# Kernel tuning notes

Measured on AMD Instinct MI355X. Metric: run time of the kernel, lower is better.

The kernel has to match this reference:

```python
import jax, jax.numpy as jnp
import numpy as np

HIDDEN = 100

def _lstm_step(h, c, gx, Whh, bhh):
    # gx: precomputed input contribution W_ih @ x + b_ih, shape [4H]
    gates = gx + Whh @ h + bhh
    i, f, g, o = jnp.split(gates, 4)
    i = jax.nn.sigmoid(i)
    f = jax.nn.sigmoid(f)
    g = jnp.tanh(g)
    o = jax.nn.sigmoid(o)
    c = f * c + i * g
    h = o * jnp.tanh(c)
    return h, c


def setup_inputs() -> dict:
    key = jax.random.key(0)
    ks = jax.random.split(key, 12)
    s = 0.1
    T_enc, T_dec = 4096, 4096
    return {
        "x": jax.random.normal(ks[0], (1, T_enc, 3), jnp.float32),
        "y": jax.random.randint(ks[1], (1, T_dec), 0, 6),
        "enc_Wih": jax.random.normal(ks[2], (4 * HIDDEN, 3), jnp.float32) * s,
        "enc_Whh": jax.random.normal(ks[3], (4 * HIDDEN, HIDDEN), jnp.float32) * s,
        "enc_bih": jax.random.normal(ks[4], (4 * HIDDEN,), jnp.float32) * s,
        "enc_bhh": jax.random.normal(ks[5], (4 * HIDDEN,), jnp.float32) * s,
        "dec_Wih": jax.random.normal(ks[6], (4 * HIDDEN, 1), jnp.float32) * s,
        "dec_Whh": jax.random.normal(ks[7], (4 * HIDDEN, HIDDEN), jnp.float32) * s,
        "dec_bih": jax.random.normal(ks[8], (4 * HIDDEN,), jnp.float32) * s,
        "dec_bhh": jax.random.normal(ks[9], (4 * HIDDEN,), jnp.float32) * s,
        "lin_W": jax.random.normal(ks[10], (6, HIDDEN), jnp.float32) * s,
        "lin_b": jax.random.normal(ks[11], (6,), jnp.float32) * s,
        "teacher_forcing_ratio": 1,
        "n_classes": 6,
    }


def reference(x, y, enc_Wih, enc_Whh, enc_bih, enc_bhh,
              dec_Wih, dec_Whh, dec_bih, dec_bhh, lin_W, lin_b,
              teacher_forcing_ratio, n_classes):
    T_dec = y.shape[1]
    # ---- Encoder: batch=1 LSTM over source sequence ----
    gx_enc = x[0] @ enc_Wih.T + enc_bih  # [T_enc, 4H]

    def enc_step(carry, gx):
        h, c = carry
        h, c = _lstm_step(h, c, gx, enc_Whh, enc_bhh)
        return (h, c), None

    h0 = jnp.zeros((HIDDEN,), x.dtype)
    (h_enc, c_enc), _ = jax.lax.scan(enc_step, (h0, h0), gx_enc)

    # ---- Decoder: single-step loop with teacher forcing ----
    yf = y[0].astype(jnp.float32)          # target labels fed as floats
    ratio = jnp.float32(teacher_forcing_ratio)
    u = jax.random.uniform(jax.random.key(1), (T_dec - 1,), jnp.float32)

    def dec_step(carry, inp):
        h, c, dec_in = carry
        u_t, y_t = inp
        gx = dec_in * dec_Wih[:, 0] + dec_bih  # scalar input -> [4H]
        h, c = _lstm_step(h, c, gx, dec_Whh, dec_bhh)
        logits = lin_W @ h + lin_b             # [n_classes]
        top_pred = jnp.argmax(logits).astype(jnp.float32)
        new_in = jnp.where(u_t < ratio, y_t, top_pred)
        return (h, c, new_in), logits

    _, logits_seq = jax.lax.scan(dec_step, (h_enc, c_enc, yf[0]), (u, yf[1:]))
    # outputs[0][t-1] = logits at step t, t = 1..T_dec-1; last row stays zero
    outputs = jnp.zeros((1, T_dec, n_classes), jnp.float32)
    outputs = outputs.at[0, : T_dec - 1].set(logits_seq)
    return outputs
```

## Files before the change

### kernel.cpp

```cpp
#include <hip/hip_runtime.h>

typedef _Float16 h2_t __attribute__((ext_vector_type(2)));

#define HID  100
#define TENC 4096
#define TDEC 4096
#define NCLS 6
#define NTHR 256

__device__ __forceinline__ float sigm(float v)  { return __builtin_amdgcn_rcpf(1.0f + __expf(-v)); }
__device__ __forceinline__ float tanh_(float v) { return 1.0f - 2.0f * __builtin_amdgcn_rcpf(1.0f + __expf(2.0f * v)); }

#define SYNC_LDS() asm volatile("s_waitcnt lgkmcnt(0)\n\ts_barrier" ::: "memory")

__device__ __forceinline__ float packh2(float a, float b) {
    h2_t p; p[0] = (_Float16)a; p[1] = (_Float16)b;
    return __builtin_bit_cast(float, p);
}

__global__ __launch_bounds__(NTHR, 1)
void lstm_rec(const float* __restrict__ x,
              const int*   __restrict__ y,
              const float* __restrict__ eWih,
              const float* __restrict__ eWhh,
              const float* __restrict__ ebih,
              const float* __restrict__ ebhh,
              const float* __restrict__ dWih,
              const float* __restrict__ dWhh,
              const float* __restrict__ dbih,
              const float* __restrict__ dbhh,
              float* __restrict__ hsto)
{
    __shared__ __align__(16) _Float16 hbuf[2][2][64];
    __shared__ __align__(8)  uint2    xst[TENC];
    __shared__               unsigned yst[TDEC];

    const int  t    = threadIdx.x;
    const int  w    = t >> 6;
    const int  l    = t & 63;
    const int  ci   = l & 31;
    const int  half = l >> 5;
    const int  cell = w * 32 + ci;
    const bool live = (cell < HID);
    const int  k0   = half * 50;

    for (int i = t; i < TENC; i += NTHR) {
        const float a = x[3*i], b = x[3*i+1], cc = x[3*i+2];
        uint2 u;
        u.x = __builtin_bit_cast(unsigned, packh2(a, b));
        u.y = __builtin_bit_cast(unsigned, packh2(cc, 1.0f));
        xst[i] = u;
    }
    for (int i = t; i < TDEC; i += NTHR)
        yst[i] = __builtin_bit_cast(unsigned, packh2((float)y[i], 0.0f));
    if (t < 256) ((_Float16*)hbuf)[t] = (_Float16)0.0f;

    float wf[4][25];
    float wxp[4][2], bs[4];
    float c = 0.0f;
    #pragma unroll
    for (int r = 0; r < 4; ++r) {
        #pragma unroll
        for (int j = 0; j < 25; ++j) wf[r][j] = 0.0f;
        wxp[r][0] = wxp[r][1] = 0.0f; bs[r] = 0.0f;
    }
    if (live) {
        #pragma unroll
        for (int r = 0; r < 4; ++r) {
            const int row = cell + r * HID;
            #pragma unroll
            for (int j = 0; j < 25; ++j)
                wf[r][j] = packh2(eWhh[row*HID + k0 + 2*j], eWhh[row*HID + k0 + 2*j + 1]);
            if (half == 0) {
                wxp[r][0] = packh2(eWih[row*3+0], eWih[row*3+1]);
                wxp[r][1] = packh2(eWih[row*3+2], 0.0f);
                bs[r]     = ebih[row] + ebhh[row];
            }
        }
    }
    __syncthreads();

    int p = 0;

    for (int s = 0; s < TENC; ++s) {
        const float4* h4 = (const float4*)&hbuf[p][half][0];
        float hp[25];
        #pragma unroll
        for (int j = 0; j < 6; ++j) {
            const float4 v = h4[j];
            hp[4*j+0] = v.x; hp[4*j+1] = v.y; hp[4*j+2] = v.z; hp[4*j+3] = v.w;
        }
        hp[24] = ((const float*)h4)[24];

        float a0, a1, a2, a3;
        if (half == 0) {
            const uint2 xp = xst[s];
            const h2_t x0 = __builtin_bit_cast(h2_t, xp.x);
            const h2_t x1 = __builtin_bit_cast(h2_t, xp.y);
            a0 = __builtin_amdgcn_fdot2(__builtin_bit_cast(h2_t, wxp[0][0]), x0,
                 __builtin_amdgcn_fdot2(__builtin_bit_cast(h2_t, wxp[0][1]), x1, bs[0], false), false);
            a1 = __builtin_amdgcn_fdot2(__builtin_bit_cast(h2_t, wxp[1][0]), x0,
                 __builtin_amdgcn_fdot2(__builtin_bit_cast(h2_t, wxp[1][1]), x1, bs[1], false), false);
            a2 = __builtin_amdgcn_fdot2(__builtin_bit_cast(h2_t, wxp[2][0]), x0,
                 __builtin_amdgcn_fdot2(__builtin_bit_cast(h2_t, wxp[2][1]), x1, bs[2], false), false);
            a3 = __builtin_amdgcn_fdot2(__builtin_bit_cast(h2_t, wxp[3][0]), x0,
                 __builtin_amdgcn_fdot2(__builtin_bit_cast(h2_t, wxp[3][1]), x1, bs[3], false), false);
        } else { a0 = a1 = a2 = a3 = 0.0f; }

        #pragma unroll
        for (int j = 0; j < 25; ++j) {
            const h2_t hh = __builtin_bit_cast(h2_t, hp[j]);
            a0 = __builtin_amdgcn_fdot2(__builtin_bit_cast(h2_t, wf[0][j]), hh, a0, false);
            a1 = __builtin_amdgcn_fdot2(__builtin_bit_cast(h2_t, wf[1][j]), hh, a1, false);
            a2 = __builtin_amdgcn_fdot2(__builtin_bit_cast(h2_t, wf[2][j]), hh, a2, false);
            a3 = __builtin_amdgcn_fdot2(__builtin_bit_cast(h2_t, wf[3][j]), hh, a3, false);
        }
        a0 += __shfl_xor(a0, 32);
        a1 += __shfl_xor(a1, 32);
        a2 += __shfl_xor(a2, 32);
        a3 += __shfl_xor(a3, 32);

        const float fi = sigm(a0), ff = sigm(a1), fg = tanh_(a2), fo = sigm(a3);
        c = ff * c + fi * fg;
        const float hn = fo * tanh_(c);
        if (half == 0 && live) {
            const int hh2 = (cell < 50) ? 0 : 1;
            hbuf[p ^ 1][hh2][cell - 50*hh2] = (_Float16)hn;
        }
        SYNC_LDS();
        p ^= 1;
    }

    float wdp[4], bsd[4];
    #pragma unroll
    for (int r = 0; r < 4; ++r) { wdp[r] = 0.0f; bsd[r] = 0.0f; }
    if (live) {
        #pragma unroll
        for (int r = 0; r < 4; ++r) {
            const int row = cell + r * HID;
            #pragma unroll
            for (int j = 0; j < 25; ++j)
                wf[r][j] = packh2(dWhh[row*HID + k0 + 2*j], dWhh[row*HID + k0 + 2*j + 1]);
            if (half == 0) {
                wdp[r] = packh2(dWih[row], 0.0f);
                bsd[r] = dbih[row] + dbhh[row];
            }
        }
    }

    for (int s = 0; s < TDEC - 1; ++s) {
        const float4* h4 = (const float4*)&hbuf[p][half][0];
        float hp[25];
        #pragma unroll
        for (int j = 0; j < 6; ++j) {
            const float4 v = h4[j];
            hp[4*j+0] = v.x; hp[4*j+1] = v.y; hp[4*j+2] = v.z; hp[4*j+3] = v.w;
        }
        hp[24] = ((const float*)h4)[24];

        float a0, a1, a2, a3;
        if (half == 0) {
            const h2_t yp = __builtin_bit_cast(h2_t, yst[s]);
            a0 = __builtin_amdgcn_fdot2(__builtin_bit_cast(h2_t, wdp[0]), yp, bsd[0], false);
            a1 = __builtin_amdgcn_fdot2(__builtin_bit_cast(h2_t, wdp[1]), yp, bsd[1], false);
            a2 = __builtin_amdgcn_fdot2(__builtin_bit_cast(h2_t, wdp[2]), yp, bsd[2], false);
            a3 = __builtin_amdgcn_fdot2(__builtin_bit_cast(h2_t, wdp[3]), yp, bsd[3], false);
        } else { a0 = a1 = a2 = a3 = 0.0f; }

        #pragma unroll
        for (int j = 0; j < 25; ++j) {
            const h2_t hh = __builtin_bit_cast(h2_t, hp[j]);
            a0 = __builtin_amdgcn_fdot2(__builtin_bit_cast(h2_t, wf[0][j]), hh, a0, false);
            a1 = __builtin_amdgcn_fdot2(__builtin_bit_cast(h2_t, wf[1][j]), hh, a1, false);
            a2 = __builtin_amdgcn_fdot2(__builtin_bit_cast(h2_t, wf[2][j]), hh, a2, false);
            a3 = __builtin_amdgcn_fdot2(__builtin_bit_cast(h2_t, wf[3][j]), hh, a3, false);
        }
        a0 += __shfl_xor(a0, 32);
        a1 += __shfl_xor(a1, 32);
        a2 += __shfl_xor(a2, 32);
        a3 += __shfl_xor(a3, 32);

        const float fi = sigm(a0), ff = sigm(a1), fg = tanh_(a2), fo = sigm(a3);
        c = ff * c + fi * fg;
        const float hn = fo * tanh_(c);
        if (live) {
            if (half == 0) {
                const int hh2 = (cell < 50) ? 0 : 1;
                hbuf[p ^ 1][hh2][cell - 50*hh2] = (_Float16)hn;
            } else {
                hsto[s * HID + cell] = hn;
            }
        }
        SYNC_LDS();
        p ^= 1;
    }
}

__global__ __launch_bounds__(256)
void logits_k(const float* __restrict__ hsto, const float* __restrict__ linW,
              const float* __restrict__ linb, float* __restrict__ out)
{
    const int idx = blockIdx.x * 256 + threadIdx.x;
    if (idx >= TDEC * NCLS) return;
    const int tt = idx / NCLS;
    const int r  = idx % NCLS;
    if (tt >= TDEC - 1) { out[idx] = 0.0f; return; }
    const float* h  = hsto + tt * HID;
    const float* wr = linW + r * HID;
    float a = linb[r];
    #pragma unroll 4
    for (int k = 0; k < HID; ++k) a += wr[k] * h[k];
    out[idx] = a;
}

extern "C" void kernel_launch(void* const* d_in, const int* in_sizes, int n_in,
                              void* d_out, int out_size, void* d_ws, size_t ws_size,
                              hipStream_t stream)
{
    const float* x    = (const float*)d_in[0];
    const int*   y    = (const int*)  d_in[1];
    const float* eWih = (const float*)d_in[2];
    const float* eWhh = (const float*)d_in[3];
    const float* ebih = (const float*)d_in[4];
    const float* ebhh = (const float*)d_in[5];
    const float* dWih = (const float*)d_in[6];
    const float* dWhh = (const float*)d_in[7];
    const float* dbih = (const float*)d_in[8];
    const float* dbhh = (const float*)d_in[9];
    const float* linW = (const float*)d_in[10];
    const float* linb = (const float*)d_in[11];
    float* out  = (float*)d_out;
    float* hsto = (float*)d_ws;

    lstm_rec<<<dim3(1), dim3(NTHR), 0, stream>>>(
        x, y, eWih, eWhh, ebih, ebhh, dWih, dWhh, dbih, dbhh, hsto);

    const int nout = TDEC * NCLS;
    logits_k<<<dim3((nout + 255) / 256), dim3(256), 0, stream>>>(hsto, linW, linb, out);
}
```

Baseline: 4.154 ms.

## Precompute LSTM input projections in a parallel kernel and prefetch per step

A new parallel kernel computes the input-gate contributions (W_ih·x plus both biases) for every encoder and decoder step, storing them as packed fp16 in workspace. The recurrent kernel loads the next step's values from global memory one step ahead and adds them on the upper-half lanes, instead of staging x and y in LDS and running extra dot products on the dependency chain. The step loop is also unrolled by two so the double-buffer index is a compile-time constant. The risk is that a one-step prefetch may not fully hide global-memory latency inside the tight serial loop. The final step also prefetches one entry past the precomputed array; that value is never used.

```diff
diff --git a/kernel.cpp b/kernel.cpp
--- a/kernel.cpp
+++ b/kernel.cpp
@@ -6,6 +6,7 @@
 #define TENC 4096
 #define TDEC 4096
 #define NCLS 6
+#define NSTEP (TENC + TDEC - 1)
 #define NTHR 256
 
 __device__ __forceinline__ float sigm(float v)  { return __builtin_amdgcn_rcpf(1.0f + __expf(-v)); }
@@ -18,22 +19,47 @@
     return __builtin_bit_cast(float, p);
 }
 
+__global__ __launch_bounds__(256)
+void gx_k(const float* __restrict__ x, const int* __restrict__ y,
+          const float* __restrict__ eWih, const float* __restrict__ ebih,
+          const float* __restrict__ ebhh, const float* __restrict__ dWih,
+          const float* __restrict__ dbih, const float* __restrict__ dbhh,
+          uint2* __restrict__ gxs)
+{
+    const int idx = blockIdx.x * 256 + threadIdx.x;
+    if (idx >= NSTEP * HID) return;
+    const int st   = idx / HID;
+    const int cell = idx - st * HID;
+    float g[4];
+    if (st < TENC) {
+        const float x0 = x[3*st], x1 = x[3*st+1], x2 = x[3*st+2];
+        #pragma unroll
+        for (int r = 0; r < 4; ++r) {
+            const int row = cell + r * HID;
+            g[r] = eWih[row*3]*x0 + eWih[row*3+1]*x1 + eWih[row*3+2]*x2
+                 + ebih[row] + ebhh[row];
+        }
+    } else {
+        const float yf = (float)y[st - TENC];
+        #pragma unroll
+        for (int r = 0; r < 4; ++r) {
+            const int row = cell + r * HID;
+            g[r] = dWih[row]*yf + dbih[row] + dbhh[row];
+        }
+    }
+    uint2 u;
+    u.x = __builtin_bit_cast(unsigned, packh2(g[0], g[1]));
+    u.y = __builtin_bit_cast(unsigned, packh2(g[2], g[3]));
+    gxs[idx] = u;
+}
+
 __global__ __launch_bounds__(NTHR, 1)
-void lstm_rec(const float* __restrict__ x,
-              const int*   __restrict__ y,
-              const float* __restrict__ eWih,
-              const float* __restrict__ eWhh,
-              const float* __restrict__ ebih,
-              const float* __restrict__ ebhh,
-              const float* __restrict__ dWih,
+void lstm_rec(const float* __restrict__ eWhh,
               const float* __restrict__ dWhh,
-              const float* __restrict__ dbih,
-              const float* __restrict__ dbhh,
+              const uint2* __restrict__ gxs,
               float* __restrict__ hsto)
 {
     __shared__ __align__(16) _Float16 hbuf[2][2][64];
-    __shared__ __align__(8)  uint2    xst[TENC];
-    __shared__               unsigned yst[TDEC];
 
     const int  t    = threadIdx.x;
     const int  w    = t >> 6;
@@ -42,28 +68,18 @@
     const int  half = l >> 5;
     const int  cell = w * 32 + ci;
     const bool live = (cell < HID);
+    const bool gldr = live && (half == 1);
     const int  k0   = half * 50;
 
-    for (int i = t; i < TENC; i += NTHR) {
-        const float a = x[3*i], b = x[3*i+1], cc = x[3*i+2];
-        uint2 u;
-        u.x = __builtin_bit_cast(unsigned, packh2(a, b));
-        u.y = __builtin_bit_cast(unsigned, packh2(cc, 1.0f));
-        xst[i] = u;
-    }
-    for (int i = t; i < TDEC; i += NTHR)
-        yst[i] = __builtin_bit_cast(unsigned, packh2((float)y[i], 0.0f));
+    float wf[4][25];
+    float c = 0.0f;
+
     if (t < 256) ((_Float16*)hbuf)[t] = (_Float16)0.0f;
 
-    float wf[4][25];
-    float wxp[4][2], bs[4];
-    float c = 0.0f;
     #pragma unroll
-    for (int r = 0; r < 4; ++r) {
+    for (int r = 0; r < 4; ++r)
         #pragma unroll
         for (int j = 0; j < 25; ++j) wf[r][j] = 0.0f;
-        wxp[r][0] = wxp[r][1] = 0.0f; bs[r] = 0.0f;
-    }
     if (live) {
         #pragma unroll
         for (int r = 0; r < 4; ++r) {
@@ -71,69 +87,59 @@
             #pragma unroll
             for (int j = 0; j < 25; ++j)
                 wf[r][j] = packh2(eWhh[row*HID + k0 + 2*j], eWhh[row*HID + k0 + 2*j + 1]);
-            if (half == 0) {
-                wxp[r][0] = packh2(eWih[row*3+0], eWih[row*3+1]);
-                wxp[r][1] = packh2(eWih[row*3+2], 0.0f);
-                bs[r]     = ebih[row] + ebhh[row];
-            }
         }
     }
     __syncthreads();
 
-    int p = 0;
-
-    for (int s = 0; s < TENC; ++s) {
-        const float4* h4 = (const float4*)&hbuf[p][half][0];
-        float hp[25];
-        #pragma unroll
-        for (int j = 0; j < 6; ++j) {
-            const float4 v = h4[j];
-            hp[4*j+0] = v.x; hp[4*j+1] = v.y; hp[4*j+2] = v.z; hp[4*j+3] = v.w;
-        }
-        hp[24] = ((const float*)h4)[24];
-
-        float a0, a1, a2, a3;
-        if (half == 0) {
-            const uint2 xp = xst[s];
-            const h2_t x0 = __builtin_bit_cast(h2_t, xp.x);
-            const h2_t x1 = __builtin_bit_cast(h2_t, xp.y);
-            a0 = __builtin_amdgcn_fdot2(__builtin_bit_cast(h2_t, wxp[0][0]), x0,
-                 __builtin_amdgcn_fdot2(__builtin_bit_cast(h2_t, wxp[0][1]), x1, bs[0], false), false);
-            a1 = __builtin_amdgcn_fdot2(__builtin_bit_cast(h2_t, wxp[1][0]), x0,
-                 __builtin_amdgcn_fdot2(__builtin_bit_cast(h2_t, wxp[1][1]), x1, bs[1], false), false);
-            a2 = __builtin_amdgcn_fdot2(__builtin_bit_cast(h2_t, wxp[2][0]), x0,
-                 __builtin_amdgcn_fdot2(__builtin_bit_cast(h2_t, wxp[2][1]), x1, bs[2], false), false);
-            a3 = __builtin_amdgcn_fdot2(__builtin_bit_cast(h2_t, wxp[3][0]), x0,
-                 __builtin_amdgcn_fdot2(__builtin_bit_cast(h2_t, wxp[3][1]), x1, bs[3], false), false);
-        } else { a0 = a1 = a2 = a3 = 0.0f; }
-
-        #pragma unroll
-        for (int j = 0; j < 25; ++j) {
-            const h2_t hh = __builtin_bit_cast(h2_t, hp[j]);
-            a0 = __builtin_amdgcn_fdot2(__builtin_bit_cast(h2_t, wf[0][j]), hh, a0, false);
-            a1 = __builtin_amdgcn_fdot2(__builtin_bit_cast(h2_t, wf[1][j]), hh, a1, false);
-            a2 = __builtin_amdgcn_fdot2(__builtin_bit_cast(h2_t, wf[2][j]), hh, a2, false);
-            a3 = __builtin_amdgcn_fdot2(__builtin_bit_cast(h2_t, wf[3][j]), hh, a3, false);
-        }
-        a0 += __shfl_xor(a0, 32);
-        a1 += __shfl_xor(a1, 32);
-        a2 += __shfl_xor(a2, 32);
-        a3 += __shfl_xor(a3, 32);
-
-        const float fi = sigm(a0), ff = sigm(a1), fg = tanh_(a2), fo = sigm(a3);
-        c = ff * c + fi * fg;
-        const float hn = fo * tanh_(c);
-        if (half == 0 && live) {
-            const int hh2 = (cell < 50) ? 0 : 1;
-            hbuf[p ^ 1][hh2][cell - 50*hh2] = (_Float16)hn;
-        }
-        SYNC_LDS();
-        p ^= 1;
-    }
-
-    float wdp[4], bsd[4];
-    #pragma unroll
-    for (int r = 0; r < 4; ++r) { wdp[r] = 0.0f; bsd[r] = 0.0f; }
+    uint2 gcur = gldr ? gxs[cell] : make_uint2(0u, 0u);
+
+    #define STEP_BODY(pin, gnext_idx, do_hsto, hsto_idx)                          \
+    {                                                                             \
+        const float4* h4 = (const float4*)&hbuf[pin][half][0];                    \
+        float hp[25];                                                             \
+        _Pragma("unroll")                                                         \
+        for (int j = 0; j < 6; ++j) {                                             \
+            const float4 v = h4[j];                                               \
+            hp[4*j+0] = v.x; hp[4*j+1] = v.y; hp[4*j+2] = v.z; hp[4*j+3] = v.w;   \
+        }                                                                         \
+        hp[24] = ((const float*)h4)[24];                                          \
+        uint2 gnew = gldr ? gxs[(gnext_idx)] : make_uint2(0u, 0u);                \
+        float a0 = 0.f, a1 = 0.f, a2 = 0.f, a3 = 0.f;                             \
+        _Pragma("unroll")                                                         \
+        for (int j = 0; j < 25; ++j) {                                            \
+            const h2_t hh = __builtin_bit_cast(h2_t, hp[j]);                      \
+            a0 = __builtin_amdgcn_fdot2(__builtin_bit_cast(h2_t, wf[0][j]), hh, a0, false); \
+            a1 = __builtin_amdgcn_fdot2(__builtin_bit_cast(h2_t, wf[1][j]), hh, a1, false); \
+            a2 = __builtin_amdgcn_fdot2(__builtin_bit_cast(h2_t, wf[2][j]), hh, a2, false); \
+            a3 = __builtin_amdgcn_fdot2(__builtin_bit_cast(h2_t, wf[3][j]), hh, a3, false); \
+        }                                                                         \
+        if (half == 1) {                                                          \
+            const h2_t g01 = __builtin_bit_cast(h2_t, gcur.x);                    \
+            const h2_t g23 = __builtin_bit_cast(h2_t, gcur.y);                    \
+            a0 += (float)g01[0]; a1 += (float)g01[1];                             \
+            a2 += (float)g23[0]; a3 += (float)g23[1];                             \
+        }                                                                         \
+        gcur = gnew;                                                              \
+        a0 += __shfl_xor(a0, 32);                                                 \
+        a1 += __shfl_xor(a1, 32);                                                 \
+        a2 += __shfl_xor(a2, 32);                                                 \
+        a3 += __shfl_xor(a3, 32);                                                 \
+        const float fi = sigm(a0), ff = sigm(a1), fg = tanh_(a2), fo = sigm(a3);  \
+        c = ff * c + fi * fg;                                                     \
+        const float hn = fo * tanh_(c);                                           \
+        if (live && half == 0) {                                                  \
+            const int hh2 = (cell < 50) ? 1 : 0;            \
+            hbuf[pin ^ 1][1 - hh2][cell - 50*(1-hh2)] = (_Float16)hn;             \
+        }                                                                         \
+        if (do_hsto && gldr) hsto[(hsto_idx) * HID + cell] = hn;                  \
+        SYNC_LDS();                                                               \
+    }
+
+    for (int s = 0; s < TENC; s += 2) {
+        STEP_BODY(0, (s + 1) * HID + cell, false, 0);
+        STEP_BODY(1, (s + 2) * HID + cell, false, 0);
+    }
+
     if (live) {
         #pragma unroll
         for (int r = 0; r < 4; ++r) {
@@ -141,59 +147,16 @@
             #pragma unroll
             for (int j = 0; j < 25; ++j)
                 wf[r][j] = packh2(dWhh[row*HID + k0 + 2*j], dWhh[row*HID + k0 + 2*j + 1]);
-            if (half == 0) {
-                wdp[r] = packh2(dWih[row], 0.0f);
-                bsd[r] = dbih[row] + dbhh[row];
-            }
-        }
-    }
-
-    for (int s = 0; s < TDEC - 1; ++s) {
-        const float4* h4 = (const float4*)&hbuf[p][half][0];
-        float hp[25];
-        #pragma unroll
-        for (int j = 0; j < 6; ++j) {
-            const float4 v = h4[j];
-            hp[4*j+0] = v.x; hp[4*j+1] = v.y; hp[4*j+2] = v.z; hp[4*j+3] = v.w;
-        }
-        hp[24] = ((const float*)h4)[24];
-
-        float a0, a1, a2, a3;
-        if (half == 0) {
-            const h2_t yp = __builtin_bit_cast(h2_t, yst[s]);
-            a0 = __builtin_amdgcn_fdot2(__builtin_bit_cast(h2_t, wdp[0]), yp, bsd[0], false);
-            a1 = __builtin_amdgcn_fdot2(__builtin_bit_cast(h2_t, wdp[1]), yp, bsd[1], false);
-            a2 = __builtin_amdgcn_fdot2(__builtin_bit_cast(h2_t, wdp[2]), yp, bsd[2], false);
-            a3 = __builtin_amdgcn_fdot2(__builtin_bit_cast(h2_t, wdp[3]), yp, bsd[3], false);
-        } else { a0 = a1 = a2 = a3 = 0.0f; }
-
-        #pragma unroll
-        for (int j = 0; j < 25; ++j) {
-            const h2_t hh = __builtin_bit_cast(h2_t, hp[j]);
-            a0 = __builtin_amdgcn_fdot2(__builtin_bit_cast(h2_t, wf[0][j]), hh, a0, false);
-            a1 = __builtin_amdgcn_fdot2(__builtin_bit_cast(h2_t, wf[1][j]), hh, a1, false);
-            a2 = __builtin_amdgcn_fdot2(__builtin_bit_cast(h2_t, wf[2][j]), hh, a2, false);
-            a3 = __builtin_amdgcn_fdot2(__builtin_bit_cast(h2_t, wf[3][j]), hh, a3, false);
-        }
-        a0 += __shfl_xor(a0, 32);
-        a1 += __shfl_xor(a1, 32);
-        a2 += __shfl_xor(a2, 32);
-        a3 += __shfl_xor(a3, 32);
-
-        const float fi = sigm(a0), ff = sigm(a1), fg = tanh_(a2), fo = sigm(a3);
-        c = ff * c + fi * fg;
-        const float hn = fo * tanh_(c);
-        if (live) {
-            if (half == 0) {
-                const int hh2 = (cell < 50) ? 0 : 1;
-                hbuf[p ^ 1][hh2][cell - 50*hh2] = (_Float16)hn;
-            } else {
-                hsto[s * HID + cell] = hn;
-            }
-        }
-        SYNC_LDS();
-        p ^= 1;
-    }
+        }
+    }
+
+    for (int s = 0; s < TDEC - 2; s += 2) {
+        STEP_BODY(0, (TENC + s + 1) * HID + cell, true, s);
+        STEP_BODY(1, (TENC + s + 2) * HID + cell, true, s + 1);
+    }
+    STEP_BODY(0, NSTEP * HID + cell, true, TDEC - 2);
+
+    #undef STEP_BODY
 }
 
 __global__ __launch_bounds__(256)
@@ -230,10 +193,15 @@
     const float* linW = (const float*)d_in[10];
     const float* linb = (const float*)d_in[11];
     float* out  = (float*)d_out;
+
     float* hsto = (float*)d_ws;
-
-    lstm_rec<<<dim3(1), dim3(NTHR), 0, stream>>>(
-        x, y, eWih, eWhh, ebih, ebhh, dWih, dWhh, dbih, dbhh, hsto);
+    uint2* gxs  = (uint2*)((char*)d_ws + (2u << 20));
+
+    const int ngx = NSTEP * HID;
+    gx_k<<<dim3((ngx + 255) / 256), dim3(256), 0, stream>>>(
+        x, y, eWih, ebih, ebhh, dWih, dbih, dbhh, gxs);
+
+    lstm_rec<<<dim3(1), dim3(NTHR), 0, stream>>>(eWhh, dWhh, gxs, hsto);
 
     const int nout = TDEC * NCLS;
     logits_k<<<dim3((nout + 255) / 256), dim3(256), 0, stream>>>(hsto, linW, linb, out);
```

Result: slower. 4.981 ms (+19.9%).

## Precompute input gate contributions in parallel kernel and prefetch per step

Applied to the files above, without the earlier changes.

Adds a parallel kernel that computes the input-side gate terms (W_ih·x + biases) for every encoder and decoder step and stores them as packed fp16 in workspace. The recurrent kernel drops its LDS staging of x/y and its per-step input dot products, and instead prefetches the next step's gate terms from global memory one step ahead, moving that work to the otherwise idle half-wave. Empty asm constraints pin the weight registers. This shortens the serial per-step critical path but adds an extra launch, a global load on every step, and fp16 rounding of the precomputed sums.

```diff
diff --git a/kernel.cpp b/kernel.cpp
--- a/kernel.cpp
+++ b/kernel.cpp
@@ -6,6 +6,7 @@
 #define TENC 4096
 #define TDEC 4096
 #define NCLS 6
+#define NSTEP (TENC + TDEC - 1)
 #define NTHR 256
 
 __device__ __forceinline__ float sigm(float v)  { return __builtin_amdgcn_rcpf(1.0f + __expf(-v)); }
@@ -18,22 +19,47 @@
     return __builtin_bit_cast(float, p);
 }
 
+__global__ __launch_bounds__(256)
+void gx_k(const float* __restrict__ x, const int* __restrict__ y,
+          const float* __restrict__ eWih, const float* __restrict__ ebih,
+          const float* __restrict__ ebhh, const float* __restrict__ dWih,
+          const float* __restrict__ dbih, const float* __restrict__ dbhh,
+          uint2* __restrict__ gxs)
+{
+    const int idx = blockIdx.x * 256 + threadIdx.x;
+    if (idx >= NSTEP * HID) return;
+    const int st   = idx / HID;
+    const int cell = idx - st * HID;
+    float g[4];
+    if (st < TENC) {
+        const float x0 = x[3*st], x1 = x[3*st+1], x2 = x[3*st+2];
+        #pragma unroll
+        for (int r = 0; r < 4; ++r) {
+            const int row = cell + r * HID;
+            g[r] = eWih[row*3]*x0 + eWih[row*3+1]*x1 + eWih[row*3+2]*x2
+                 + ebih[row] + ebhh[row];
+        }
+    } else {
+        const float yf = (float)y[st - TENC];
+        #pragma unroll
+        for (int r = 0; r < 4; ++r) {
+            const int row = cell + r * HID;
+            g[r] = dWih[row]*yf + dbih[row] + dbhh[row];
+        }
+    }
+    uint2 u;
+    u.x = __builtin_bit_cast(unsigned, packh2(g[0], g[1]));
+    u.y = __builtin_bit_cast(unsigned, packh2(g[2], g[3]));
+    gxs[idx] = u;
+}
+
 __global__ __launch_bounds__(NTHR, 1)
-void lstm_rec(const float* __restrict__ x,
-              const int*   __restrict__ y,
-              const float* __restrict__ eWih,
-              const float* __restrict__ eWhh,
-              const float* __restrict__ ebih,
-              const float* __restrict__ ebhh,
-              const float* __restrict__ dWih,
+void lstm_rec(const float* __restrict__ eWhh,
               const float* __restrict__ dWhh,
-              const float* __restrict__ dbih,
-              const float* __restrict__ dbhh,
+              const uint2* __restrict__ gxs,
               float* __restrict__ hsto)
 {
     __shared__ __align__(16) _Float16 hbuf[2][2][64];
-    __shared__ __align__(8)  uint2    xst[TENC];
-    __shared__               unsigned yst[TDEC];
 
     const int  t    = threadIdx.x;
     const int  w    = t >> 6;
@@ -42,28 +68,18 @@
     const int  half = l >> 5;
     const int  cell = w * 32 + ci;
     const bool live = (cell < HID);
+    const bool gldr = live && (half == 1);
     const int  k0   = half * 50;
 
-    for (int i = t; i < TENC; i += NTHR) {
-        const float a = x[3*i], b = x[3*i+1], cc = x[3*i+2];
-        uint2 u;
-        u.x = __builtin_bit_cast(unsigned, packh2(a, b));
-        u.y = __builtin_bit_cast(unsigned, packh2(cc, 1.0f));
-        xst[i] = u;
-    }
-    for (int i = t; i < TDEC; i += NTHR)
-        yst[i] = __builtin_bit_cast(unsigned, packh2((float)y[i], 0.0f));
+    float wf[4][25];
+    float c = 0.0f;
+
     if (t < 256) ((_Float16*)hbuf)[t] = (_Float16)0.0f;
 
-    float wf[4][25];
-    float wxp[4][2], bs[4];
-    float c = 0.0f;
     #pragma unroll
-    for (int r = 0; r < 4; ++r) {
+    for (int r = 0; r < 4; ++r)
         #pragma unroll
         for (int j = 0; j < 25; ++j) wf[r][j] = 0.0f;
-        wxp[r][0] = wxp[r][1] = 0.0f; bs[r] = 0.0f;
-    }
     if (live) {
         #pragma unroll
         for (int r = 0; r < 4; ++r) {
@@ -71,15 +87,16 @@
             #pragma unroll
             for (int j = 0; j < 25; ++j)
                 wf[r][j] = packh2(eWhh[row*HID + k0 + 2*j], eWhh[row*HID + k0 + 2*j + 1]);
-            if (half == 0) {
-                wxp[r][0] = packh2(eWih[row*3+0], eWih[row*3+1]);
-                wxp[r][1] = packh2(eWih[row*3+2], 0.0f);
-                bs[r]     = ebih[row] + ebhh[row];
-            }
-        }
-    }
+        }
+    }
+    #pragma unroll
+    for (int r = 0; r < 4; ++r)
+        #pragma unroll
+        for (int j = 0; j < 25; ++j)
+            asm volatile("" : "+v"(wf[r][j]));
     __syncthreads();
 
+    uint2 gcur = gldr ? gxs[cell] : make_uint2(0u, 0u);
     int p = 0;
 
     for (int s = 0; s < TENC; ++s) {
@@ -93,19 +110,14 @@
         hp[24] = ((const float*)h4)[24];
 
         float a0, a1, a2, a3;
-        if (half == 0) {
-            const uint2 xp = xst[s];
-            const h2_t x0 = __builtin_bit_cast(h2_t, xp.x);
-            const h2_t x1 = __builtin_bit_cast(h2_t, xp.y);
-            a0 = __builtin_amdgcn_fdot2(__builtin_bit_cast(h2_t, wxp[0][0]), x0,
-                 __builtin_amdgcn_fdot2(__builtin_bit_cast(h2_t, wxp[0][1]), x1, bs[0], false), false);
-            a1 = __builtin_amdgcn_fdot2(__builtin_bit_cast(h2_t, wxp[1][0]), x0,
-                 __builtin_amdgcn_fdot2(__builtin_bit_cast(h2_t, wxp[1][1]), x1, bs[1], false), false);
-            a2 = __builtin_amdgcn_fdot2(__builtin_bit_cast(h2_t, wxp[2][0]), x0,
-                 __builtin_amdgcn_fdot2(__builtin_bit_cast(h2_t, wxp[2][1]), x1, bs[2], false), false);
-            a3 = __builtin_amdgcn_fdot2(__builtin_bit_cast(h2_t, wxp[3][0]), x0,
-                 __builtin_amdgcn_fdot2(__builtin_bit_cast(h2_t, wxp[3][1]), x1, bs[3], false), false);
+        if (half == 1) {
+            const h2_t g01 = __builtin_bit_cast(h2_t, gcur.x);
+            const h2_t g23 = __builtin_bit_cast(h2_t, gcur.y);
+            a0 = (float)g01[0]; a1 = (float)g01[1];
+            a2 = (float)g23[0]; a3 = (float)g23[1];
         } else { a0 = a1 = a2 = a3 = 0.0f; }
+
+        uint2 gnew = gldr ? gxs[(s + 1) * HID + cell] : make_uint2(0u, 0u);
 
         #pragma unroll
         for (int j = 0; j < 25; ++j) {
@@ -115,6 +127,8 @@
             a2 = __builtin_amdgcn_fdot2(__builtin_bit_cast(h2_t, wf[2][j]), hh, a2, false);
             a3 = __builtin_amdgcn_fdot2(__builtin_bit_cast(h2_t, wf[3][j]), hh, a3, false);
         }
+        gcur = gnew;
+
         a0 += __shfl_xor(a0, 32);
         a1 += __shfl_xor(a1, 32);
         a2 += __shfl_xor(a2, 32);
@@ -131,9 +145,6 @@
         p ^= 1;
     }
 
-    float wdp[4], bsd[4];
-    #pragma unroll
-    for (int r = 0; r < 4; ++r) { wdp[r] = 0.0f; bsd[r] = 0.0f; }
     if (live) {
         #pragma unroll
         for (int r = 0; r < 4; ++r) {
@@ -141,12 +152,13 @@
             #pragma unroll
             for (int j = 0; j < 25; ++j)
                 wf[r][j] = packh2(dWhh[row*HID + k0 + 2*j], dWhh[row*HID + k0 + 2*j + 1]);
-            if (half == 0) {
-                wdp[r] = packh2(dWih[row], 0.0f);
-                bsd[r] = dbih[row] + dbhh[row];
-            }
-        }
-    }
+        }
+    }
+    #pragma unroll
+    for (int r = 0; r < 4; ++r)
+        #pragma unroll
+        for (int j = 0; j < 25; ++j)
+            asm volatile("" : "+v"(wf[r][j]));
 
     for (int s = 0; s < TDEC - 1; ++s) {
         const float4* h4 = (const float4*)&hbuf[p][half][0];
@@ -159,13 +171,14 @@
         hp[24] = ((const float*)h4)[24];
 
         float a0, a1, a2, a3;
-        if (half == 0) {
-            const h2_t yp = __builtin_bit_cast(h2_t, yst[s]);
-            a0 = __builtin_amdgcn_fdot2(__builtin_bit_cast(h2_t, wdp[0]), yp, bsd[0], false);
-            a1 = __builtin_amdgcn_fdot2(__builtin_bit_cast(h2_t, wdp[1]), yp, bsd[1], false);
-            a2 = __builtin_amdgcn_fdot2(__builtin_bit_cast(h2_t, wdp[2]), yp, bsd[2], false);
-            a3 = __builtin_amdgcn_fdot2(__builtin_bit_cast(h2_t, wdp[3]), yp, bsd[3], false);
+        if (half == 1) {
+            const h2_t g01 = __builtin_bit_cast(h2_t, gcur.x);
+            const h2_t g23 = __builtin_bit_cast(h2_t, gcur.y);
+            a0 = (float)g01[0]; a1 = (float)g01[1];
+            a2 = (float)g23[0]; a3 = (float)g23[1];
         } else { a0 = a1 = a2 = a3 = 0.0f; }
+
+        uint2 gnew = gldr ? gxs[(TENC + s + 1) * HID + cell] : make_uint2(0u, 0u);
 
         #pragma unroll
         for (int j = 0; j < 25; ++j) {
@@ -175,6 +188,8 @@
             a2 = __builtin_amdgcn_fdot2(__builtin_bit_cast(h2_t, wf[2][j]), hh, a2, false);
             a3 = __builtin_amdgcn_fdot2(__builtin_bit_cast(h2_t, wf[3][j]), hh, a3, false);
         }
+        gcur = gnew;
+
         a0 += __shfl_xor(a0, 32);
         a1 += __shfl_xor(a1, 32);
         a2 += __shfl_xor(a2, 32);
@@ -230,10 +245,15 @@
     const float* linW = (const float*)d_in[10];
     const float* linb = (const float*)d_in[11];
     float* out  = (float*)d_out;
+
     float* hsto = (float*)d_ws;
-
-    lstm_rec<<<dim3(1), dim3(NTHR), 0, stream>>>(
-        x, y, eWih, eWhh, ebih, ebhh, dWih, dWhh, dbih, dbhh, hsto);
+    uint2* gxs  = (uint2*)((char*)d_ws + (2u << 20));
+
+    const int ngx = NSTEP * HID;
+    gx_k<<<dim3((ngx + 255) / 256), dim3(256), 0, stream>>>(
+        x, y, eWih, ebih, ebhh, dWih, dbih, dbhh, gxs);
+
+    lstm_rec<<<dim3(1), dim3(NTHR), 0, stream>>>(eWhh, dWhh, gxs, hsto);
 
     const int nout = TDEC * NCLS;
     logits_k<<<dim3((nout + 255) / 256), dim3(256), 0, stream>>>(hsto, linW, linb, out);
```

Result: slower. 5.100 ms (+22.8%).
